# Kernel optimization log

Hardware: AMD Instinct MI355X
Metric: run time of the kernel (lower is better)

Reference implementation:

```python
import jax, jax.numpy as jnp
import numpy as np

DIM = 1024
DEPTH = 6
HEADS = 16
MLP = 4096
HEAD_DIM = DIM // HEADS
SCALE = HEAD_DIM ** -0.5
EPS = 1e-5


def _ln(x, g, b):
    m = jnp.mean(x, axis=-1, keepdims=True)
    v = jnp.mean(jnp.square(x - m), axis=-1, keepdims=True)
    return (x - m) * jax.lax.rsqrt(v + EPS) * g + b


def setup_inputs() -> dict:
    key = jax.random.key(0)
    ks = jax.random.split(key, 16)
    B, N = 4, 1024
    s_d = 1.0 / np.sqrt(DIM)
    s_m = 1.0 / np.sqrt(MLP)
    inp = {
        "x1": jax.random.normal(ks[0], (B, N, DIM), jnp.float32),
        "x2": jax.random.normal(ks[1], (B, N, DIM), jnp.float32),
        # stacked per-layer params; Linear weights stored as [in, out]
        "ln1_g": jnp.ones((DEPTH, DIM), jnp.float32),
        "ln1_b": jnp.zeros((DEPTH, DIM), jnp.float32),
        "wq": jax.random.normal(ks[2], (DEPTH, DIM, DIM), jnp.float32) * s_d,
        "wk": jax.random.normal(ks[3], (DEPTH, DIM, DIM), jnp.float32) * s_d,
        "wv": jax.random.normal(ks[4], (DEPTH, DIM, DIM), jnp.float32) * s_d,
        "wo": jax.random.normal(ks[5], (DEPTH, DIM, DIM), jnp.float32) * s_d,
        "bo": jnp.zeros((DEPTH, DIM), jnp.float32),
        "ln2_g": jnp.ones((DEPTH, DIM), jnp.float32),
        "ln2_b": jnp.zeros((DEPTH, DIM), jnp.float32),
        "w1": jax.random.normal(ks[6], (DEPTH, DIM, MLP), jnp.float32) * s_d,
        "b1": jnp.zeros((DEPTH, MLP), jnp.float32),
        "w2": jax.random.normal(ks[7], (DEPTH, MLP, DIM), jnp.float32) * s_m,
        "b2": jnp.zeros((DEPTH, DIM), jnp.float32),
    }
    return inp


def _split_heads(t):
    b, n, _ = t.shape
    return t.reshape(b, n, HEADS, HEAD_DIM).transpose(0, 2, 1, 3)  # b h n d


def reference(x1, x2, ln1_g, ln1_b, wq, wk, wv, wo, bo, ln2_g, ln2_b, w1, b1, w2, b2):
    # dropout disabled (eval mode)
    for i in range(DEPTH):
        # PreNorm(MCA): same LayerNorm params applied to x1 and x2
        n1 = _ln(x1, ln1_g[i], ln1_b[i])
        n2 = _ln(x2, ln1_g[i], ln1_b[i])
        q = _split_heads(n1 @ wq[i])
        k = _split_heads(n2 @ wk[i])
        v = _split_heads(n2 @ wv[i])
        dots = jnp.einsum('bhqd,bhkd->bhqk', q, k) * SCALE
        attn = jax.nn.softmax(dots, axis=-1)
        out = jnp.einsum('bhqk,bhkd->bhqd', attn, v)
        b, h, n, d = out.shape
        out = out.transpose(0, 2, 1, 3).reshape(b, n, h * d)
        x1 = out @ wo[i] + bo[i] + x1
        # PreNorm(FeedForward)
        nf = _ln(x1, ln2_g[i], ln2_b[i])
        hdn = jax.nn.gelu(nf @ w1[i] + b1[i], approximate=False)
        x1 = hdn @ w2[i] + b2[i] + x1
    return x1
```

## Files before the change

kernel.cpp:

```cpp
#include <hip/hip_runtime.h>
#include <stdint.h>

#define N_SEQ 1024
#define N_TOK 4096
#define ATT_SCALE 0.125f

typedef unsigned short u16;
typedef __attribute__((ext_vector_type(8))) short short8;
typedef __attribute__((ext_vector_type(4))) short short4v;
typedef __attribute__((ext_vector_type(4))) float f32x4;

__device__ __forceinline__ u16 f2bf(float f) {
  uint32_t u = __float_as_uint(f);
  u += 0x7fffu + ((u >> 16) & 1u);
  return (u16)(u >> 16);
}

__device__ __forceinline__ void gload16(const void* g, void* lds) {
  __builtin_amdgcn_global_load_lds(
      (const __attribute__((address_space(1))) unsigned int*)g,
      (__attribute__((address_space(3))) unsigned int*)lds, 16, 0, 0);
}

__global__ void copy_f32_kernel(const float* __restrict__ in, float* __restrict__ out) {
  int i = blockIdx.x * 256 + threadIdx.x;
  ((float4*)out)[i] = ((const float4*)in)[i];
}

__global__ __launch_bounds__(256) void tconv_kernel(const float* __restrict__ src,
                                                    u16* __restrict__ dst,
                                                    int K, int NN, size_t dstLS) {
  __shared__ u16 tile[64][68];
  int n0 = blockIdx.x * 64, k0 = blockIdx.y * 64, L = blockIdx.z;
  const float* s = src + (size_t)L * K * NN;
  u16* d = dst + (size_t)L * dstLS;
  int t = threadIdx.x;
  int rr = t >> 4, cc = (t & 15) * 4;
#pragma unroll
  for (int ii = 0; ii < 4; ii++) {
    int kl = rr + ii * 16;
    float4 v = *(const float4*)&s[(size_t)(k0 + kl) * NN + n0 + cc];
    tile[cc + 0][kl] = f2bf(v.x);
    tile[cc + 1][kl] = f2bf(v.y);
    tile[cc + 2][kl] = f2bf(v.z);
    tile[cc + 3][kl] = f2bf(v.w);
  }
  __syncthreads();
#pragma unroll
  for (int ii = 0; ii < 4; ii++) {
    int nl = rr + ii * 16;
    short4v o;
    o.x = (short)tile[nl][cc + 0];
    o.y = (short)tile[nl][cc + 1];
    o.z = (short)tile[nl][cc + 2];
    o.w = (short)tile[nl][cc + 3];
    *(short4v*)&d[(size_t)(n0 + nl) * K + k0 + cc] = o;
  }
}

__global__ __launch_bounds__(256) void ln_kernel(const float* __restrict__ x,
                                                 const float* __restrict__ g,
                                                 const float* __restrict__ b,
                                                 u16* __restrict__ out) {
  int row = blockIdx.x;
  const float* xr = x + (size_t)row * 1024;
  int t = threadIdx.x;
  float4 v = *(const float4*)&xr[t * 4];
  float s = v.x + v.y + v.z + v.w;
  float sq = v.x * v.x + v.y * v.y + v.z * v.z + v.w * v.w;
#pragma unroll
  for (int m = 1; m < 64; m <<= 1) {
    s += __shfl_xor(s, m, 64);
    sq += __shfl_xor(sq, m, 64);
  }
  __shared__ float ps[8];
  int w = t >> 6;
  if ((t & 63) == 0) { ps[w] = s; ps[4 + w] = sq; }
  __syncthreads();
  s = ps[0] + ps[1] + ps[2] + ps[3];
  sq = ps[4] + ps[5] + ps[6] + ps[7];
  float mean = s * (1.0f / 1024.0f);
  float var = sq * (1.0f / 1024.0f) - mean * mean;
  float rs = rsqrtf(var + 1e-5f);
  float4 gv = *(const float4*)&g[t * 4];
  float4 bv = *(const float4*)&b[t * 4];
  short4v o;
  o.x = (short)f2bf((v.x - mean) * rs * gv.x + bv.x);
  o.y = (short)f2bf((v.y - mean) * rs * gv.y + bv.y);
  o.z = (short)f2bf((v.z - mean) * rs * gv.z + bv.z);
  o.w = (short)f2bf((v.w - mean) * rs * gv.w + bv.w);
  *(short4v*)&out[(size_t)row * 1024 + t * 4] = o;
}

template <int BM, int BN, int WM, int WN, int MODE>
__global__ __launch_bounds__(WM * WN * 64, 2) void gemm8(const u16* __restrict__ A,
                                                         const u16* __restrict__ Bt,
                                                         u16* __restrict__ outb,
                                                         float* __restrict__ outf,
                                                         const float* __restrict__ bias,
                                                         const float* __restrict__ resid,
                                                         int N, int K) {
  constexpr int BK = 64;
  constexpr int NW = WM * WN;
  constexpr int T = NW * 64;
  constexpr int WTM = BM / WM, WTN = BN / WN;
  constexpr int FM = WTM / 16, FN = WTN / 16, HM = FM / 2;
  constexpr int AT = BM * BK, BTL = BN * BK;
  constexpr int LA = AT / 8 / T, LB = BTL / 8 / T;
  constexpr int LTOT = LA + LB;
  __shared__ u16 smem[2 * (AT + BTL)];

  int t = threadIdx.x, lane = t & 63, w = t >> 6;
  int wm = w / WN, wn = w % WN;
  const u16* Ag = A + (size_t)(blockIdx.y * BM) * K;
  const u16* Bg = Bt + (size_t)(blockIdx.x * BN) * K;
  f32x4 acc[FM][FN] = {};

  auto stage = [&](int d, int k0) {
    u16* ab = smem + d * (AT + BTL);
    u16* bb = ab + AT;
#pragma unroll
    for (int l = 0; l < LA; l++) {
      int c = (l * NW + w) * 64 + lane;
      int r = c >> 3, s = c & 7;
      gload16(Ag + (size_t)r * K + k0 + ((s ^ (r & 7)) << 3), ab + (l * NW + w) * 512);
    }
#pragma unroll
    for (int l = 0; l < LB; l++) {
      int c = (l * NW + w) * 64 + lane;
      int r = c >> 3, s = c & 7;
      gload16(Bg + (size_t)r * K + k0 + ((s ^ (r & 7)) << 3), bb + (l * NW + w) * 512);
    }
  };

  auto rdA = [&](const u16* ab, int mi, int ks) {
    int rr = wm * WTM + mi * 16 + (lane & 15);
    int j = ks * 4 + (lane >> 4);
    return *(const short8*)&ab[rr * BK + ((j ^ (rr & 7)) << 3)];
  };
  auto rdB = [&](const u16* bb, int ni, int ks) {
    int rr = wn * WTN + ni * 16 + (lane & 15);
    int j = ks * 4 + (lane >> 4);
    return *(const short8*)&bb[rr * BK + ((j ^ (rr & 7)) << 3)];
  };

  const int NT = K / BK;
  stage(0, 0);
  stage(1, BK);
  __builtin_amdgcn_sched_barrier(0);

  int buf = 0;
  for (int tt = 0; tt < NT; tt++) {
    asm volatile("s_waitcnt vmcnt(%0)" ::"n"(LTOT) : "memory");
    __builtin_amdgcn_s_barrier();
    __builtin_amdgcn_sched_barrier(0);
    const u16* ab = smem + buf * (AT + BTL);
    const u16* bb = ab + AT;
    short8 b0[FN], a0lo[HM], a0hi[HM], b1[FN], a1lo[HM], a1hi[HM];
#pragma unroll
    for (int n = 0; n < FN; n++) b0[n] = rdB(bb, n, 0);
#pragma unroll
    for (int m = 0; m < HM; m++) a0lo[m] = rdA(ab, m, 0);
#pragma unroll
    for (int m = 0; m < HM; m++) a0hi[m] = rdA(ab, HM + m, 0);
    asm volatile("s_waitcnt lgkmcnt(%0)" ::"n"(HM) : "memory");
    __builtin_amdgcn_sched_barrier(0);
#pragma unroll
    for (int n = 0; n < FN; n++) b1[n] = rdB(bb, n, 1);
#pragma unroll
    for (int m = 0; m < HM; m++) a1lo[m] = rdA(ab, m, 1);
    __builtin_amdgcn_s_setprio(1);
#pragma unroll
    for (int m = 0; m < HM; m++)
#pragma unroll
      for (int n = 0; n < FN; n++)
        acc[m][n] = __builtin_amdgcn_mfma_f32_16x16x32_bf16(a0lo[m], b0[n], acc[m][n], 0, 0, 0);
    __builtin_amdgcn_s_setprio(0);
    asm volatile("s_waitcnt lgkmcnt(%0)" ::"n"(FN + HM) : "memory");
    __builtin_amdgcn_sched_barrier(0);
#pragma unroll
    for (int m = 0; m < HM; m++) a1hi[m] = rdA(ab, HM + m, 1);
    __builtin_amdgcn_s_setprio(1);
#pragma unroll
    for (int m = 0; m < HM; m++)
#pragma unroll
      for (int n = 0; n < FN; n++)
        acc[HM + m][n] = __builtin_amdgcn_mfma_f32_16x16x32_bf16(a0hi[m], b0[n], acc[HM + m][n], 0, 0, 0);
    __builtin_amdgcn_s_setprio(0);
    asm volatile("s_waitcnt lgkmcnt(%0)" ::"n"(HM) : "memory");
    __builtin_amdgcn_sched_barrier(0);
    __builtin_amdgcn_s_setprio(1);
#pragma unroll
    for (int m = 0; m < HM; m++)
#pragma unroll
      for (int n = 0; n < FN; n++)
        acc[m][n] = __builtin_amdgcn_mfma_f32_16x16x32_bf16(a1lo[m], b1[n], acc[m][n], 0, 0, 0);
    __builtin_amdgcn_s_setprio(0);
    asm volatile("s_waitcnt lgkmcnt(0)" ::: "memory");
    __builtin_amdgcn_sched_barrier(0);
    __builtin_amdgcn_s_barrier();
    __builtin_amdgcn_sched_barrier(0);
    stage(buf, ((tt + 2) % NT) * BK);
    __builtin_amdgcn_sched_barrier(0);
    __builtin_amdgcn_s_setprio(1);
#pragma unroll
    for (int m = 0; m < HM; m++)
#pragma unroll
      for (int n = 0; n < FN; n++)
        acc[HM + m][n] = __builtin_amdgcn_mfma_f32_16x16x32_bf16(a1hi[m], b1[n], acc[HM + m][n], 0, 0, 0);
    __builtin_amdgcn_s_setprio(0);
    buf ^= 1;
  }

  int r0 = blockIdx.y * BM + wm * WTM + ((lane >> 4) << 2);
  int c0 = blockIdx.x * BN + wn * WTN + (lane & 15);
#pragma unroll
  for (int mi = 0; mi < FM; mi++) {
#pragma unroll
    for (int r = 0; r < 4; r++) {
      size_t row = (size_t)(r0 + mi * 16 + r);
#pragma unroll
      for (int ni = 0; ni < FN; ni++) {
        size_t col = (size_t)(c0 + ni * 16);
        size_t idx = row * N + col;
        float val = acc[mi][ni][r];
        if (MODE == 0) {
          outb[idx] = f2bf(val);
        } else if (MODE == 1) {
          outf[idx] = val + bias[col] + resid[idx];
        } else {
          float xg = val + bias[col];
          outb[idx] = f2bf(0.5f * xg * (1.0f + erff(xg * 0.70710678f)));
        }
      }
    }
  }
}

__global__ __launch_bounds__(256) void attn_kernel(const u16* __restrict__ qb,
                                                   const u16* __restrict__ kvb,
                                                   u16* __restrict__ ob) {
  int qt = blockIdx.x, bh = blockIdx.y;
  int b = bh >> 4, h = bh & 15;
  int t = threadIdx.x, lane = t & 63, w = t >> 6;
  __shared__ u16 Qs[64 * 64];
  __shared__ u16 Ks[64 * 64];
  __shared__ u16 Vt[64 * 64];
  __shared__ u16 Ps[4][16 * 64];

  const u16* qbase = qb + (size_t)b * N_SEQ * 1024 + h * 64;
  const u16* kbase = kvb + (size_t)b * N_SEQ * 2048 + h * 64;
  const u16* vbase = kbase + 1024;
  u16* obase = ob + (size_t)b * N_SEQ * 1024 + h * 64;

  {
    int r = t >> 2, c = (t & 3) * 16;
    const u16* src = qbase + (size_t)(qt * 64 + r) * 1024 + c;
    *(short8*)&Qs[r * 64 + c] = *(const short8*)src;
    *(short8*)&Qs[r * 64 + c + 8] = *(const short8*)(src + 8);
  }
  __syncthreads();
  short8 qa0 = *(const short8*)&Qs[(w * 16 + (lane & 15)) * 64 + (lane >> 4) * 8];
  short8 qa1 = *(const short8*)&Qs[(w * 16 + (lane & 15)) * 64 + 32 + (lane >> 4) * 8];

  f32x4 o[4] = {};
  float m_r[4] = {-1e30f, -1e30f, -1e30f, -1e30f};
  float l_r[4] = {0.0f, 0.0f, 0.0f, 0.0f};

  for (int kt = 0; kt < 16; kt++) {
    __syncthreads();
    {
      int r = t >> 2, c = (t & 3) * 16;
      const u16* ksrc = kbase + (size_t)(kt * 64 + r) * 2048 + c;
      *(short8*)&Ks[r * 64 + c] = *(const short8*)ksrc;
      *(short8*)&Ks[r * 64 + c + 8] = *(const short8*)(ksrc + 8);
      const u16* vsrc = vbase + (size_t)(kt * 64 + r) * 2048 + c;
      short8 v0 = *(const short8*)vsrc;
      short8 v1 = *(const short8*)(vsrc + 8);
#pragma unroll
      for (int j = 0; j < 8; j++) {
        Vt[(c + j) * 64 + r] = (u16)v0[j];
        Vt[(c + 8 + j) * 64 + r] = (u16)v1[j];
      }
    }
    __syncthreads();

    f32x4 s[4] = {};
#pragma unroll
    for (int kb = 0; kb < 4; kb++) {
      short8 k0 = *(const short8*)&Ks[(kb * 16 + (lane & 15)) * 64 + (lane >> 4) * 8];
      short8 k1 = *(const short8*)&Ks[(kb * 16 + (lane & 15)) * 64 + 32 + (lane >> 4) * 8];
      s[kb] = __builtin_amdgcn_mfma_f32_16x16x32_bf16(qa0, k0, s[kb], 0, 0, 0);
      s[kb] = __builtin_amdgcn_mfma_f32_16x16x32_bf16(qa1, k1, s[kb], 0, 0, 0);
    }
    float fac[4], rowsum[4];
#pragma unroll
    for (int r = 0; r < 4; r++) {
      float a = fmaxf(fmaxf(s[0][r], s[1][r]), fmaxf(s[2][r], s[3][r])) * ATT_SCALE;
      a = fmaxf(a, __shfl_xor(a, 1, 64));
      a = fmaxf(a, __shfl_xor(a, 2, 64));
      a = fmaxf(a, __shfl_xor(a, 4, 64));
      a = fmaxf(a, __shfl_xor(a, 8, 64));
      float mn = fmaxf(m_r[r], a);
      fac[r] = __expf(m_r[r] - mn);
      m_r[r] = mn;
      rowsum[r] = 0.0f;
    }
#pragma unroll
    for (int kb = 0; kb < 4; kb++) {
#pragma unroll
      for (int r = 0; r < 4; r++) {
        float p = __expf(s[kb][r] * ATT_SCALE - m_r[r]);
        rowsum[r] += p;
        Ps[w][((lane >> 4) * 4 + r) * 64 + kb * 16 + (lane & 15)] = f2bf(p);
      }
    }
#pragma unroll
    for (int r = 0; r < 4; r++) {
      float rs = rowsum[r];
      rs += __shfl_xor(rs, 1, 64);
      rs += __shfl_xor(rs, 2, 64);
      rs += __shfl_xor(rs, 4, 64);
      rs += __shfl_xor(rs, 8, 64);
      l_r[r] = l_r[r] * fac[r] + rs;
      o[0][r] *= fac[r];
      o[1][r] *= fac[r];
      o[2][r] *= fac[r];
      o[3][r] *= fac[r];
    }
    __syncthreads();
#pragma unroll
    for (int ks = 0; ks < 2; ks++) {
      short8 pf = *(const short8*)&Ps[w][(lane & 15) * 64 + ks * 32 + (lane >> 4) * 8];
#pragma unroll
      for (int db = 0; db < 4; db++) {
        short8 vf = *(const short8*)&Vt[(db * 16 + (lane & 15)) * 64 + ks * 32 + (lane >> 4) * 8];
        o[db] = __builtin_amdgcn_mfma_f32_16x16x32_bf16(pf, vf, o[db], 0, 0, 0);
      }
    }
  }
#pragma unroll
  for (int r = 0; r < 4; r++) {
    float inv = 1.0f / l_r[r];
    size_t row = (size_t)(qt * 64 + w * 16 + (lane >> 4) * 4 + r);
#pragma unroll
    for (int db = 0; db < 4; db++)
      obase[row * 1024 + db * 16 + (lane & 15)] = f2bf(o[db][r] * inv);
  }
}

extern "C" void kernel_launch(void* const* d_in, const int* in_sizes, int n_in,
                              void* d_out, int out_size, void* d_ws, size_t ws_size,
                              hipStream_t stream) {
  const float* x1 = (const float*)d_in[0];
  const float* x2 = (const float*)d_in[1];
  const float* ln1_g = (const float*)d_in[2];
  const float* ln1_b = (const float*)d_in[3];
  const float* wq = (const float*)d_in[4];
  const float* wk = (const float*)d_in[5];
  const float* wv = (const float*)d_in[6];
  const float* wo = (const float*)d_in[7];
  const float* bo = (const float*)d_in[8];
  const float* ln2_g = (const float*)d_in[9];
  const float* ln2_b = (const float*)d_in[10];
  const float* w1 = (const float*)d_in[11];
  const float* b1 = (const float*)d_in[12];
  const float* w2 = (const float*)d_in[13];
  const float* b2 = (const float*)d_in[14];
  float* xout = (float*)d_out;

  u16* p = (u16*)d_ws;
  u16* wqt = p;  p += (size_t)6 * 1024 * 1024;
  u16* kvt = p;  p += (size_t)6 * 2048 * 1024;
  u16* wot = p;  p += (size_t)6 * 1024 * 1024;
  u16* w1t = p;  p += (size_t)6 * 4096 * 1024;
  u16* w2t = p;  p += (size_t)6 * 1024 * 4096;
  u16* n1 = p;   p += (size_t)N_TOK * 1024;
  u16* n2 = p;   p += (size_t)N_TOK * 1024;
  u16* qbuf = p; p += (size_t)N_TOK * 1024;
  u16* kvbuf = p; p += (size_t)N_TOK * 2048;
  u16* ao = p;   p += (size_t)N_TOK * 1024;
  u16* hid = p;  p += (size_t)N_TOK * 4096;

  dim3 blk(256);
  tconv_kernel<<<dim3(16, 16, 6), blk, 0, stream>>>(wq, wqt, 1024, 1024, (size_t)1024 * 1024);
  tconv_kernel<<<dim3(16, 16, 6), blk, 0, stream>>>(wk, kvt, 1024, 1024, (size_t)2048 * 1024);
  tconv_kernel<<<dim3(16, 16, 6), blk, 0, stream>>>(wv, kvt + (size_t)1024 * 1024, 1024, 1024, (size_t)2048 * 1024);
  tconv_kernel<<<dim3(16, 16, 6), blk, 0, stream>>>(wo, wot, 1024, 1024, (size_t)1024 * 1024);
  tconv_kernel<<<dim3(64, 16, 6), blk, 0, stream>>>(w1, w1t, 1024, 4096, (size_t)4096 * 1024);
  tconv_kernel<<<dim3(16, 64, 6), blk, 0, stream>>>(w2, w2t, 4096, 1024, (size_t)1024 * 4096);
  copy_f32_kernel<<<4096, blk, 0, stream>>>(x1, xout);

  for (int i = 0; i < 6; i++) {
    ln_kernel<<<N_TOK, blk, 0, stream>>>(xout, ln1_g + i * 1024, ln1_b + i * 1024, n1);
    ln_kernel<<<N_TOK, blk, 0, stream>>>(x2, ln1_g + i * 1024, ln1_b + i * 1024, n2);
    gemm8<128, 128, 2, 2, 0><<<dim3(8, 32), dim3(256), 0, stream>>>(
        n1, wqt + (size_t)i * 1024 * 1024, qbuf, nullptr, nullptr, nullptr, 1024, 1024);
    gemm8<128, 128, 2, 2, 0><<<dim3(16, 32), dim3(256), 0, stream>>>(
        n2, kvt + (size_t)i * 2048 * 1024, kvbuf, nullptr, nullptr, nullptr, 2048, 1024);
    attn_kernel<<<dim3(16, 64), blk, 0, stream>>>(qbuf, kvbuf, ao);
    gemm8<128, 128, 2, 2, 1><<<dim3(8, 32), dim3(256), 0, stream>>>(
        ao, wot + (size_t)i * 1024 * 1024, nullptr, xout, bo + i * 1024, xout, 1024, 1024);
    ln_kernel<<<N_TOK, blk, 0, stream>>>(xout, ln2_g + i * 1024, ln2_b + i * 1024, n1);
    gemm8<256, 256, 2, 4, 2><<<dim3(16, 16), dim3(512), 0, stream>>>(
        n1, w1t + (size_t)i * 4096 * 1024, hid, nullptr, b1 + i * 4096, nullptr, 4096, 1024);
    gemm8<128, 128, 2, 2, 1><<<dim3(8, 32), dim3(256), 0, stream>>>(
        hid, w2t + (size_t)i * 1024 * 4096, nullptr, xout, b2 + i * 1024, xout, 1024, 4096);
  }
}
```

Measured before the change: 1.823 ms.

## Swizzle attention LDS, prefetch K/V into registers, retune GEMM tiles

The attention kernel now XOR-swizzles the K, transposed V and P tiles in shared memory to cut bank conflicts. It loads the next K/V tile into registers while the current tile is being computed, and it removes one barrier per iteration. Separately, the Q, O-projection and FFN2 GEMMs switch to 128x64 tiles and FFN1 to 128x128 tiles, raising the block count on the 256-CU device. Occupancy hints are added to the attention launch bounds. The trade-off is more register pressure and smaller tiles that reuse each loaded operand less.

Measured after the change: 1.581 ms. -13.3%, faster.

```diff
diff --git a/kernel.cpp b/kernel.cpp
--- a/kernel.cpp
+++ b/kernel.cpp
@@ -237,9 +237,9 @@
   }
 }
 
-__global__ __launch_bounds__(256) void attn_kernel(const u16* __restrict__ qb,
-                                                   const u16* __restrict__ kvb,
-                                                   u16* __restrict__ ob) {
+__global__ __launch_bounds__(256, 4) void attn_kernel(const u16* __restrict__ qb,
+                                                      const u16* __restrict__ kvb,
+                                                      u16* __restrict__ ob) {
   int qt = blockIdx.x, bh = blockIdx.y;
   int b = bh >> 4, h = bh & 15;
   int t = threadIdx.x, lane = t & 63, w = t >> 6;
@@ -253,12 +253,21 @@
   const u16* vbase = kbase + 1024;
   u16* obase = ob + (size_t)b * N_SEQ * 1024 + h * 64;
 
+  int r = t >> 2, c = (t & 3) * 16;
   {
-    int r = t >> 2, c = (t & 3) * 16;
     const u16* src = qbase + (size_t)(qt * 64 + r) * 1024 + c;
     *(short8*)&Qs[r * 64 + c] = *(const short8*)src;
     *(short8*)&Qs[r * 64 + c + 8] = *(const short8*)(src + 8);
   }
+  short8 kreg0, kreg1, vreg0, vreg1;
+  {
+    const u16* ksrc = kbase + (size_t)r * 2048 + c;
+    kreg0 = *(const short8*)ksrc;
+    kreg1 = *(const short8*)(ksrc + 8);
+    const u16* vsrc = vbase + (size_t)r * 2048 + c;
+    vreg0 = *(const short8*)vsrc;
+    vreg1 = *(const short8*)(vsrc + 8);
+  }
   __syncthreads();
   short8 qa0 = *(const short8*)&Qs[(w * 16 + (lane & 15)) * 64 + (lane >> 4) * 8];
   short8 qa1 = *(const short8*)&Qs[(w * 16 + (lane & 15)) * 64 + 32 + (lane >> 4) * 8];
@@ -268,84 +277,95 @@
   float l_r[4] = {0.0f, 0.0f, 0.0f, 0.0f};
 
   for (int kt = 0; kt < 16; kt++) {
+    if (kt > 0) __syncthreads();
+    {
+      int jj0 = c >> 3;
+      *(short8*)&Ks[r * 64 + ((jj0 ^ (r & 7)) << 3)] = kreg0;
+      *(short8*)&Ks[r * 64 + (((jj0 + 1) ^ (r & 7)) << 3)] = kreg1;
+#pragma unroll
+      for (int j = 0; j < 8; j++) {
+        int row = c + j, rowb = c + 8 + j;
+        Vt[row * 64 + (((r >> 3) ^ (row & 7)) << 3) + (r & 7)] = (u16)vreg0[j];
+        Vt[rowb * 64 + (((r >> 3) ^ (rowb & 7)) << 3) + (r & 7)] = (u16)vreg1[j];
+      }
+    }
     __syncthreads();
-    {
-      int r = t >> 2, c = (t & 3) * 16;
-      const u16* ksrc = kbase + (size_t)(kt * 64 + r) * 2048 + c;
-      *(short8*)&Ks[r * 64 + c] = *(const short8*)ksrc;
-      *(short8*)&Ks[r * 64 + c + 8] = *(const short8*)(ksrc + 8);
-      const u16* vsrc = vbase + (size_t)(kt * 64 + r) * 2048 + c;
-      short8 v0 = *(const short8*)vsrc;
-      short8 v1 = *(const short8*)(vsrc + 8);
-#pragma unroll
-      for (int j = 0; j < 8; j++) {
-        Vt[(c + j) * 64 + r] = (u16)v0[j];
-        Vt[(c + 8 + j) * 64 + r] = (u16)v1[j];
-      }
-    }
-    __syncthreads();
+    if (kt < 15) {
+      const u16* ksrc = kbase + (size_t)((kt + 1) * 64 + r) * 2048 + c;
+      kreg0 = *(const short8*)ksrc;
+      kreg1 = *(const short8*)(ksrc + 8);
+      const u16* vsrc = vbase + (size_t)((kt + 1) * 64 + r) * 2048 + c;
+      vreg0 = *(const short8*)vsrc;
+      vreg1 = *(const short8*)(vsrc + 8);
+    }
 
     f32x4 s[4] = {};
 #pragma unroll
     for (int kb = 0; kb < 4; kb++) {
-      short8 k0 = *(const short8*)&Ks[(kb * 16 + (lane & 15)) * 64 + (lane >> 4) * 8];
-      short8 k1 = *(const short8*)&Ks[(kb * 16 + (lane & 15)) * 64 + 32 + (lane >> 4) * 8];
+      int key = kb * 16 + (lane & 15);
+      int jj = lane >> 4;
+      short8 k0 = *(const short8*)&Ks[key * 64 + ((jj ^ (key & 7)) << 3)];
+      short8 k1 = *(const short8*)&Ks[key * 64 + (((4 + jj) ^ (key & 7)) << 3)];
       s[kb] = __builtin_amdgcn_mfma_f32_16x16x32_bf16(qa0, k0, s[kb], 0, 0, 0);
       s[kb] = __builtin_amdgcn_mfma_f32_16x16x32_bf16(qa1, k1, s[kb], 0, 0, 0);
     }
     float fac[4], rowsum[4];
 #pragma unroll
-    for (int r = 0; r < 4; r++) {
-      float a = fmaxf(fmaxf(s[0][r], s[1][r]), fmaxf(s[2][r], s[3][r])) * ATT_SCALE;
+    for (int rr = 0; rr < 4; rr++) {
+      float a = fmaxf(fmaxf(s[0][rr], s[1][rr]), fmaxf(s[2][rr], s[3][rr])) * ATT_SCALE;
       a = fmaxf(a, __shfl_xor(a, 1, 64));
       a = fmaxf(a, __shfl_xor(a, 2, 64));
       a = fmaxf(a, __shfl_xor(a, 4, 64));
       a = fmaxf(a, __shfl_xor(a, 8, 64));
-      float mn = fmaxf(m_r[r], a);
-      fac[r] = __expf(m_r[r] - mn);
-      m_r[r] = mn;
-      rowsum[r] = 0.0f;
+      float mn = fmaxf(m_r[rr], a);
+      fac[rr] = __expf(m_r[rr] - mn);
+      m_r[rr] = mn;
+      rowsum[rr] = 0.0f;
     }
 #pragma unroll
     for (int kb = 0; kb < 4; kb++) {
-#pragma unroll
-      for (int r = 0; r < 4; r++) {
-        float p = __expf(s[kb][r] * ATT_SCALE - m_r[r]);
-        rowsum[r] += p;
-        Ps[w][((lane >> 4) * 4 + r) * 64 + kb * 16 + (lane & 15)] = f2bf(p);
+      int chunk = 2 * kb + ((lane & 15) >> 3);
+#pragma unroll
+      for (int rr = 0; rr < 4; rr++) {
+        float p = __expf(s[kb][rr] * ATT_SCALE - m_r[rr]);
+        rowsum[rr] += p;
+        int row = (lane >> 4) * 4 + rr;
+        Ps[w][row * 64 + ((chunk ^ (row & 7)) << 3) + (lane & 7)] = f2bf(p);
       }
     }
 #pragma unroll
-    for (int r = 0; r < 4; r++) {
-      float rs = rowsum[r];
+    for (int rr = 0; rr < 4; rr++) {
+      float rs = rowsum[rr];
       rs += __shfl_xor(rs, 1, 64);
       rs += __shfl_xor(rs, 2, 64);
       rs += __shfl_xor(rs, 4, 64);
       rs += __shfl_xor(rs, 8, 64);
-      l_r[r] = l_r[r] * fac[r] + rs;
-      o[0][r] *= fac[r];
-      o[1][r] *= fac[r];
-      o[2][r] *= fac[r];
-      o[3][r] *= fac[r];
-    }
-    __syncthreads();
+      l_r[rr] = l_r[rr] * fac[rr] + rs;
+      o[0][rr] *= fac[rr];
+      o[1][rr] *= fac[rr];
+      o[2][rr] *= fac[rr];
+      o[3][rr] *= fac[rr];
+    }
 #pragma unroll
     for (int ks = 0; ks < 2; ks++) {
-      short8 pf = *(const short8*)&Ps[w][(lane & 15) * 64 + ks * 32 + (lane >> 4) * 8];
+      int rowp = lane & 15;
+      int jj = 4 * ks + (lane >> 4);
+      short8 pf = *(const short8*)&Ps[w][rowp * 64 + ((jj ^ (rowp & 7)) << 3)];
 #pragma unroll
       for (int db = 0; db < 4; db++) {
-        short8 vf = *(const short8*)&Vt[(db * 16 + (lane & 15)) * 64 + ks * 32 + (lane >> 4) * 8];
+        int row = db * 16 + (lane & 15);
+        short8 vf = *(const short8*)&Vt[row * 64 + ((jj ^ (row & 7)) << 3)];
         o[db] = __builtin_amdgcn_mfma_f32_16x16x32_bf16(pf, vf, o[db], 0, 0, 0);
       }
     }
   }
 #pragma unroll
-  for (int r = 0; r < 4; r++) {
-    float inv = 1.0f / l_r[r];
-    size_t row = (size_t)(qt * 64 + w * 16 + (lane >> 4) * 4 + r);
+  for (int rr = 0; rr < 4; rr++) {
+    float inv = 1.0f / l_r[rr];
+    size_t row = (size_t)(qt * 64 + w * 16 + (lane >> 4) * 4 + rr);
 #pragma unroll
     for (int db = 0; db < 4; db++)
-      obase[row * 1024 + db * 16 + (lane & 15)] = f2bf(o[db][r] * inv);
+      obase[row * 1024 + db * 16 + (lane & 15)] = f2bf(o[db][rr] * inv);
   }
 }
 
@@ -394,17 +414,17 @@
   for (int i = 0; i < 6; i++) {
     ln_kernel<<<N_TOK, blk, 0, stream>>>(xout, ln1_g + i * 1024, ln1_b + i * 1024, n1);
     ln_kernel<<<N_TOK, blk, 0, stream>>>(x2, ln1_g + i * 1024, ln1_b + i * 1024, n2);
-    gemm8<128, 128, 2, 2, 0><<<dim3(8, 32), dim3(256), 0, stream>>>(
+    gemm8<128, 64, 2, 2, 0><<<dim3(16, 32), dim3(256), 0, stream>>>(
         n1, wqt + (size_t)i * 1024 * 1024, qbuf, nullptr, nullptr, nullptr, 1024, 1024);
     gemm8<128, 128, 2, 2, 0><<<dim3(16, 32), dim3(256), 0, stream>>>(
         n2, kvt + (size_t)i * 2048 * 1024, kvbuf, nullptr, nullptr, nullptr, 2048, 1024);
     attn_kernel<<<dim3(16, 64), blk, 0, stream>>>(qbuf, kvbuf, ao);
-    gemm8<128, 128, 2, 2, 1><<<dim3(8, 32), dim3(256), 0, stream>>>(
+    gemm8<128, 64, 2, 2, 1><<<dim3(16, 32), dim3(256), 0, stream>>>(
         ao, wot + (size_t)i * 1024 * 1024, nullptr, xout, bo + i * 1024, xout, 1024, 1024);
     ln_kernel<<<N_TOK, blk, 0, stream>>>(xout, ln2_g + i * 1024, ln2_b + i * 1024, n1);
-    gemm8<256, 256, 2, 4, 2><<<dim3(16, 16), dim3(512), 0, stream>>>(
+    gemm8<128, 128, 2, 2, 2><<<dim3(32, 32), dim3(256), 0, stream>>>(
         n1, w1t + (size_t)i * 4096 * 1024, hid, nullptr, b1 + i * 4096, nullptr, 4096, 1024);
-    gemm8<128, 128, 2, 2, 1><<<dim3(8, 32), dim3(256), 0, stream>>>(
+    gemm8<128, 64, 2, 2, 1><<<dim3(16, 32), dim3(256), 0, stream>>>(
         hid, w2t + (size_t)i * 1024 * 4096, nullptr, xout, b2 + i * 1024, xout, 1024, 4096);
   }
 }
```
